# Performance work log

Hardware: AMD Instinct MI355X
Metric: run time of the kernel (lower is better)

The kernel has to match this reference:

```python
import jax, jax.numpy as jnp
import numpy as np

B, S, V = 2, 336, 8      # batch, seq_len, n_vars
D, H, P = 256, 8, 96     # d_model, num_heads, pred_len
DK = D // H
OUT_CHN = 8
EPS = 1e-5


def _layernorm(x, g, b):
    mu = jnp.mean(x, axis=-1, keepdims=True)
    var = jnp.var(x, axis=-1, keepdims=True)
    return (x - mu) * jax.lax.rsqrt(var + EPS) * g + b


def _attn_ff(src, Wq, bq, Wk, bk, Wv, bv, Wo, bo, ln1_g, ln1_b):
    # src: [N, L, D]; manual MHA + residual + layernorm (dropout=0)
    N, L, _ = src.shape
    q = (src @ Wq + bq).reshape(N, L, H, DK).transpose(0, 2, 1, 3)
    k = (src @ Wk + bk).reshape(N, L, H, DK).transpose(0, 2, 1, 3)
    v = (src @ Wv + bv).reshape(N, L, H, DK).transpose(0, 2, 1, 3)
    scores = jnp.einsum('nhqd,nhkd->nhqk', q, k) / np.sqrt(DK).astype(np.float32)
    attn = jax.nn.softmax(scores, axis=-1)
    o = jnp.einsum('nhqk,nhkd->nhqd', attn, v)
    o = o.transpose(0, 2, 1, 3).reshape(N, L, D) @ Wo + bo
    return _layernorm(src + o, ln1_g, ln1_b)


def setup_inputs() -> dict:
    key = jax.random.key(0)
    ks = jax.random.split(key, 8)
    s = 1.0 / np.sqrt(D)
    return {
        'x': jax.random.normal(ks[0], (B, S, V), dtype=jnp.float32),
        'emb_w': jax.random.normal(ks[1], (1, D), dtype=jnp.float32),
        'emb_b': jnp.zeros((D,), jnp.float32),
        'Wq': jax.random.normal(ks[2], (D, D), dtype=jnp.float32) * s,
        'bq': jnp.zeros((D,), jnp.float32),
        'Wk': jax.random.normal(ks[3], (D, D), dtype=jnp.float32) * s,
        'bk': jnp.zeros((D,), jnp.float32),
        'Wv': jax.random.normal(ks[4], (D, D), dtype=jnp.float32) * s,
        'bv': jnp.zeros((D,), jnp.float32),
        'Wo': jax.random.normal(ks[5], (D, D), dtype=jnp.float32) * s,
        'bo': jnp.zeros((D,), jnp.float32),
        'ln1_g': jnp.ones((D,), jnp.float32),
        'ln1_b': jnp.zeros((D,), jnp.float32),
        'norm_g': jnp.ones((D,), jnp.float32),
        'norm_b': jnp.zeros((D,), jnp.float32),
        'proj_w': jax.random.normal(ks[6], (S * D, P), dtype=jnp.float32) / np.sqrt(S * D).astype(np.float32),
        'proj_b': jnp.zeros((P,), jnp.float32),
    }


def reference(x, emb_w, emb_b, Wq, bq, Wk, bk, Wv, bv, Wo, bo,
              ln1_g, ln1_b, norm_g, norm_b, proj_w, proj_b):
    attn_p = (Wq, bq, Wk, bk, Wv, bv, Wo, bo, ln1_g, ln1_b)
    # x: [B,S,V] -> [B,V,S] -> embed each scalar to D
    e = x.transpose(0, 2, 1)[..., None] @ emb_w + emb_b  # [B,V,S,D]
    for _ in range(10):
        # attention over time axis (shared weights)
        e = _attn_ff(e.reshape(B * V, S, D), *attn_p).reshape(B, V, S, D)
        e = _layernorm(e.transpose(0, 2, 1, 3), norm_g, norm_b)  # [B,S,V,D]
        # attention over variable axis (same weights)
        e = _attn_ff(e.reshape(B * S, V, D), *attn_p).reshape(B, S, V, D)
        e = e.transpose(0, 2, 1, 3)  # [B,V,S,D]
    out = e.reshape(B, V, S * D) @ proj_w + proj_b  # [B,V,P]
    return out.transpose(0, 2, 1)[:, :, :OUT_CHN]  # [B,P,out_chn]
```

## Files before the change

### kernel.cpp

```cpp
#include <hip/hip_runtime.h>

#define SS 336
#define VV 8
#define DD 256
#define DKK 32
#define NTOK 5376
#define NTD (NTOK * DD)
#define ATT_SCALE 0.17677669529663687f
#define LN_EPS 1e-5f

typedef _Float16 f16x8 __attribute__((ext_vector_type(8)));
typedef _Float16 f16x4v __attribute__((ext_vector_type(4)));
typedef __attribute__((ext_vector_type(4))) float f32x4;

__device__ inline _Float16 f2h(float f) { return (_Float16)f; }

__global__ __launch_bounds__(256) void k_prep_w(
    const float* __restrict__ Wq, const float* __restrict__ Wk,
    const float* __restrict__ Wv, const float* __restrict__ Wo,
    _Float16* __restrict__ WT2) {
  int z = blockIdx.y;
  const float* W = (z == 0) ? Wq : (z == 1) ? Wk : (z == 2) ? Wv : Wo;
  int o = blockIdx.x * 256 + threadIdx.x;
  int blk = o >> 9;
  int idx = o & 511;
  int lane = idx >> 3, j = idx & 7;
  int nt = blk >> 3, kb = blk & 7;
  int lcol = lane & 15, quad = lane >> 4;
  int n = nt * 16 + lcol;
  int k = kb * 32 + quad * 8 + j;
  WT2[(size_t)z * 65536 + o] = f2h(W[k * 256 + n]);
}

__global__ __launch_bounds__(256) void k_embed(
    const float* __restrict__ x, const float* __restrict__ ew,
    const float* __restrict__ eb, float* __restrict__ E,
    _Float16* __restrict__ E16) {
  int token = blockIdx.x;
  int n = token / SS, s = token - n * SS;
  int b = n >> 3, v = n & 7;
  float xv = x[(b * SS + s) * VV + v];
  int d = threadIdx.x;
  float val = fmaf(xv, ew[d], eb[d]);
  E[token * DD + d] = val;
  E16[token * DD + d] = f2h(val);
}

__global__ __launch_bounds__(256) void k_gemm_qkv(
    const _Float16* __restrict__ A16, const _Float16* __restrict__ WT2,
    const float* __restrict__ c0, const float* __restrict__ c1,
    const float* __restrict__ c2,
    _Float16* __restrict__ H0, _Float16* __restrict__ H1,
    _Float16* __restrict__ H2) {
  int z = blockIdx.z;
  const float* bias = (z == 0) ? c0 : (z == 1) ? c1 : c2;
  _Float16* H       = (z == 0) ? H0 : (z == 1) ? H1 : H2;
  int m0 = blockIdx.x * 64;
  int tid = threadIdx.x;
  int wave = tid >> 6, lane = tid & 63;
  int wm = wave >> 1, wn = wave & 1;
  int quad = lane >> 4, lcol = lane & 15;
  int ntb = blockIdx.y * 8 + wn * 4;

  __shared__ _Float16 As[4 * 64 * 8];

  f32x4 acc[2][4] = {};

  for (int kb = 0; kb < 8; ++kb) {
    int k0 = kb * 32;
    __syncthreads();
    {
      int row = tid >> 2, ks = tid & 3;
      *(f16x8*)&As[(ks * 64 + row) * 8] =
          *(const f16x8*)&A16[(size_t)(m0 + row) * 256 + k0 + ks * 8];
    }
    __syncthreads();
    f16x8 af[2];
#pragma unroll
    for (int mt = 0; mt < 2; ++mt)
      af[mt] = *(const f16x8*)&As[(quad * 64 + wm * 32 + mt * 16 + lcol) * 8];
#pragma unroll
    for (int nt = 0; nt < 4; ++nt) {
      f16x8 bfr = *(const f16x8*)&WT2[(size_t)z * 65536 +
                                      ((ntb + nt) * 8 + kb) * 512 + lane * 8];
#pragma unroll
      for (int mt = 0; mt < 2; ++mt)
        acc[mt][nt] = __builtin_amdgcn_mfma_f32_16x16x32_f16(
            af[mt], bfr, acc[mt][nt], 0, 0, 0);
    }
  }

  float bsv[4];
#pragma unroll
  for (int nt = 0; nt < 4; ++nt) bsv[nt] = bias[(ntb + nt) * 16 + lcol];
#pragma unroll
  for (int mt = 0; mt < 2; ++mt) {
#pragma unroll
    for (int i = 0; i < 4; ++i) {
      int r = m0 + wm * 32 + mt * 16 + quad * 4 + i;
#pragma unroll
      for (int nt = 0; nt < 4; ++nt) {
        int c = (ntb + nt) * 16 + lcol;
        H[(size_t)r * 256 + c] = f2h(acc[mt][nt][i] + bsv[nt]);
      }
    }
  }
}

#define KSTR 36
#define VTSTR 344
__global__ __launch_bounds__(512) void k_attn_time(
    const _Float16* __restrict__ Q, const _Float16* __restrict__ K,
    const _Float16* __restrict__ V, _Float16* __restrict__ O16) {
  int qg = blockIdx.x, h = blockIdx.y, n = blockIdx.z;
  int tid = threadIdx.x;
  int wave = tid >> 6, lane = tid & 63;
  int quad = lane >> 4, lcol = lane & 15;

  __shared__ _Float16 Ks[336 * KSTR];
  __shared__ _Float16 Vt[32 * VTSTR + 16];
  __shared__ _Float16 Ps[8][16 * 40];

  const size_t base = (size_t)(n * SS) * DD + h * DKK;

  for (int c = tid; c < 1344; c += 512) {
    int row = c >> 2, part = c & 3;
    f16x8 kv = *(const f16x8*)&K[base + (size_t)row * DD + part * 8];
    f16x4v klo = __builtin_shufflevector(kv, kv, 0, 1, 2, 3);
    f16x4v khi = __builtin_shufflevector(kv, kv, 4, 5, 6, 7);
    *(f16x4v*)&Ks[row * KSTR + part * 8] = klo;
    *(f16x4v*)&Ks[row * KSTR + part * 8 + 4] = khi;
    f16x8 vv = *(const f16x8*)&V[base + (size_t)row * DD + part * 8];
#pragma unroll
    for (int j = 0; j < 8; ++j) Vt[(part * 8 + j) * VTSTR + row] = vv[j];
  }
  for (int c = tid; c < 272; c += 512) {
    if (c < 256) {
      int d = c >> 3, col = 336 + (c & 7);
      Vt[d * VTSTR + col] = (_Float16)0.f;
    } else {
      Vt[32 * VTSTR + (c - 256)] = (_Float16)0.f;
    }
  }
  __syncthreads();

  _Float16* P = Ps[wave];
  const f16x8 onesv = {(_Float16)1.f, (_Float16)1.f, (_Float16)1.f, (_Float16)1.f,
                       (_Float16)1.f, (_Float16)1.f, (_Float16)1.f, (_Float16)1.f};
  const f32x4 z4 = {0.f, 0.f, 0.f, 0.f};

  int qt0 = qg ? 11 : 0;
  int qtend = qg ? 21 : 11;
  for (int qtile = qt0 + wave; qtile < qtend; qtile += 8) {
    int qb = qtile * 16;

    f16x8 qf = *(const f16x8*)&Q[base + (size_t)(qb + lcol) * DD + quad * 8];
    f32x4 accA = {0.f, 0.f, 0.f, 0.f};
    f32x4 accB = {0.f, 0.f, 0.f, 0.f};
    f32x4 lacc = {0.f, 0.f, 0.f, 0.f};
    float m_[4] = {-1e30f, -1e30f, -1e30f, -1e30f};

    for (int t = 0; t < 11; ++t) {
      int k0 = t * 32;
      bool full = (t < 10);
      const _Float16* kp0 = &Ks[(k0 + lcol) * KSTR + quad * 8];
      f16x4v ka = *(const f16x4v*)kp0;
      f16x4v kb = *(const f16x4v*)(kp0 + 4);
      f16x8 kf0 = __builtin_shufflevector(ka, kb, 0, 1, 2, 3, 4, 5, 6, 7);
      f32x4 s0 = __builtin_amdgcn_mfma_f32_16x16x32_f16(qf, kf0, z4, 0, 0, 0);
      f32x4 s1 = z4;
      if (full) {
        const _Float16* kp1 = &Ks[(k0 + 16 + lcol) * KSTR + quad * 8];
        f16x4v ka1 = *(const f16x4v*)kp1;
        f16x4v kb1 = *(const f16x4v*)(kp1 + 4);
        f16x8 kf1 = __builtin_shufflevector(ka1, kb1, 0, 1, 2, 3, 4, 5, 6, 7);
        s1 = __builtin_amdgcn_mfma_f32_16x16x32_f16(qf, kf1, z4, 0, 0, 0);
      }
      float sc0[4], sc1[4], p0[4], p1[4], corr[4];
#pragma unroll
      for (int i = 0; i < 4; ++i) {
        sc0[i] = s0[i] * ATT_SCALE;
        sc1[i] = full ? s1[i] * ATT_SCALE : -1e30f;
      }
#pragma unroll
      for (int i = 0; i < 4; ++i) {
        float t2 = fmaxf(sc0[i], sc1[i]);
        t2 = fmaxf(t2, __shfl_xor(t2, 1));
        t2 = fmaxf(t2, __shfl_xor(t2, 2));
        t2 = fmaxf(t2, __shfl_xor(t2, 4));
        t2 = fmaxf(t2, __shfl_xor(t2, 8));
        float nm = fmaxf(m_[i], t2);
        corr[i] = __expf(m_[i] - nm);
        m_[i] = nm;
        p0[i] = __expf(sc0[i] - nm);
        p1[i] = __expf(sc1[i] - nm);
        accA[i] *= corr[i];
        accB[i] *= corr[i];
        lacc[i] *= corr[i];
      }
#pragma unroll
      for (int i = 0; i < 4; ++i) {
        P[(quad * 4 + i) * 40 + lcol] = f2h(p0[i]);
        P[(quad * 4 + i) * 40 + 16 + lcol] = f2h(p1[i]);
      }
      f16x8 pf = *(const f16x8*)&P[lcol * 40 + quad * 8];
      lacc = __builtin_amdgcn_mfma_f32_16x16x32_f16(pf, onesv, lacc, 0, 0, 0);
      f16x8 vb0 = *(const f16x8*)&Vt[lcol * VTSTR + k0 + quad * 8];
      f16x8 vb1 = *(const f16x8*)&Vt[(16 + lcol) * VTSTR + k0 + quad * 8];
      accA = __builtin_amdgcn_mfma_f32_16x16x32_f16(pf, vb0, accA, 0, 0, 0);
      accB = __builtin_amdgcn_mfma_f32_16x16x32_f16(pf, vb1, accB, 0, 0, 0);
    }

#pragma unroll
    for (int i = 0; i < 4; ++i) {
      float inv = 1.f / lacc[i];
      P[(quad * 4 + i) * 40 + lcol] = f2h(accA[i] * inv);
      P[(quad * 4 + i) * 40 + 16 + lcol] = f2h(accB[i] * inv);
    }
    int row = lane >> 2, seg = lane & 3;
    f16x8 ov = *(const f16x8*)&P[row * 40 + seg * 8];
    *(f16x8*)&O16[base + (size_t)(qb + row) * DD + seg * 8] = ov;
  }
}

__global__ __launch_bounds__(512) void k_mega_var(
    const _Float16* __restrict__ AO16, const _Float16* __restrict__ WT2,
    const float* __restrict__ bq, const float* __restrict__ bk,
    const float* __restrict__ bv, const float* __restrict__ bo,
    const float* __restrict__ g1, const float* __restrict__ c1,
    const float* __restrict__ gn, const float* __restrict__ bn,
    float* __restrict__ Etime, _Float16* __restrict__ Q16,
    _Float16* __restrict__ K16, _Float16* __restrict__ V16, int doqkv) {
  int tid = threadIdx.x;
  int wave = tid >> 6, lane = tid & 63;
  int quad = lane >> 4, lcol = lane & 15;

  __shared__ int rmapS[32];
  __shared__ _Float16 Af[32 * 264];
  __shared__ float Cf[32 * 260];
  __shared__ _Float16 QKVs[32 * 776];

  if (tid < 32) {
    int r2 = blockIdx.x * 32 + tid;
    int n_idx = r2 >> 3, v = r2 & 7;
    int b = n_idx / SS, s = n_idx - b * SS;
    rmapS[tid] = (b * VV + v) * SS + s;
  }
  __syncthreads();

  {
    int row = tid >> 4, seg = tid & 15;
    const _Float16* src = AO16 + (size_t)rmapS[row] * DD + seg * 16;
    _Float16* dst = Af + row * 264 + seg * 16;
    *(f16x8*)(dst) = *(const f16x8*)(src);
    *(f16x8*)(dst + 8) = *(const f16x8*)(src + 8);
  }
  __syncthreads();

  const _Float16* WoF = WT2 + (size_t)3 * 65536;

  {
    f32x4 acc[2][2] = {};
    for (int kb = 0; kb < 8; ++kb) {
      int k0 = kb * 32;
      f16x8 af0 = *(const f16x8*)&Af[lcol * 264 + k0 + quad * 8];
      f16x8 af1 = *(const f16x8*)&Af[(16 + lcol) * 264 + k0 + quad * 8];
#pragma unroll
      for (int nt = 0; nt < 2; ++nt) {
        f16x8 bfr = *(const f16x8*)&WoF[((wave * 2 + nt) * 8 + kb) * 512 + lane * 8];
        acc[0][nt] = __builtin_amdgcn_mfma_f32_16x16x32_f16(af0, bfr, acc[0][nt], 0, 0, 0);
        acc[1][nt] = __builtin_amdgcn_mfma_f32_16x16x32_f16(af1, bfr, acc[1][nt], 0, 0, 0);
      }
    }
#pragma unroll
    for (int mt = 0; mt < 2; ++mt) {
#pragma unroll
      for (int i = 0; i < 4; ++i) {
        int row = mt * 16 + quad * 4 + i;
        size_t rb = (size_t)rmapS[row] * 256;
#pragma unroll
        for (int nt = 0; nt < 2; ++nt) {
          int col = (wave * 2 + nt) * 16 + lcol;
          Cf[row * 260 + col] = acc[mt][nt][i] + bo[col] + Etime[rb + col];
        }
      }
    }
  }
  __syncthreads();

  {
    int row = tid >> 4, c0 = (tid & 15) * 16;
    float v[16];
#pragma unroll
    for (int j = 0; j < 16; ++j) v[j] = Cf[row * 260 + c0 + j];
#pragma unroll
    for (int pass = 0; pass < 2; ++pass) {
      const float* gg = pass ? gn : g1;
      const float* bb = pass ? bn : c1;
      float s = 0.f, q = 0.f;
#pragma unroll
      for (int j = 0; j < 16; ++j) { s += v[j]; q = fmaf(v[j], v[j], q); }
      s += __shfl_xor(s, 1); q += __shfl_xor(q, 1);
      s += __shfl_xor(s, 2); q += __shfl_xor(q, 2);
      s += __shfl_xor(s, 4); q += __shfl_xor(q, 4);
      s += __shfl_xor(s, 8); q += __shfl_xor(q, 8);
      float mu = s * (1.0f / 256.0f);
      float rs = rsqrtf(q * (1.0f / 256.0f) - mu * mu + LN_EPS);
#pragma unroll
      for (int j = 0; j < 16; ++j)
        v[j] = fmaf((v[j] - mu) * rs, gg[c0 + j], bb[c0 + j]);
    }
#pragma unroll
    for (int j = 0; j < 16; ++j) Cf[row * 260 + c0 + j] = v[j];
#pragma unroll
    for (int j8 = 0; j8 < 2; ++j8) {
      f16x8 h;
#pragma unroll
      for (int jj = 0; jj < 8; ++jj) h[jj] = f2h(v[j8 * 8 + jj]);
      *(f16x8*)&Af[row * 264 + c0 + j8 * 8] = h;
    }
  }
  __syncthreads();

  {
    f32x4 acc[2][6] = {};
    for (int kb = 0; kb < 8; ++kb) {
      int k0 = kb * 32;
      f16x8 af0 = *(const f16x8*)&Af[lcol * 264 + k0 + quad * 8];
      f16x8 af1 = *(const f16x8*)&Af[(16 + lcol) * 264 + k0 + quad * 8];
#pragma unroll
      for (int j = 0; j < 6; ++j) {
        int ntg = wave * 6 + j;
        f16x8 bfr = *(const f16x8*)&WT2[(size_t)(ntg * 8 + kb) * 512 + lane * 8];
        acc[0][j] = __builtin_amdgcn_mfma_f32_16x16x32_f16(af0, bfr, acc[0][j], 0, 0, 0);
        acc[1][j] = __builtin_amdgcn_mfma_f32_16x16x32_f16(af1, bfr, acc[1][j], 0, 0, 0);
      }
    }
#pragma unroll
    for (int j = 0; j < 6; ++j) {
      int ntg = wave * 6 + j;
      int colb = ntg * 16;
      int z = colb >> 8, coln = (colb & 255) + lcol;
      const float* bz = (z == 0) ? bq : (z == 1) ? bk : bv;
      float bval = bz[coln];
#pragma unroll
      for (int mt = 0; mt < 2; ++mt) {
#pragma unroll
        for (int i = 0; i < 4; ++i)
          QKVs[(mt * 16 + quad * 4 + i) * 776 + colb + lcol] = f2h(acc[mt][j][i] + bval);
      }
    }
  }
  __syncthreads();

  if (tid < 256) {
    int ng = tid >> 6, h = (tid >> 3) & 7, qi = tid & 7;
    const _Float16* Qp = &QKVs[(ng * 8 + qi) * 776 + h * 32];
    float qv[32];
#pragma unroll
    for (int j4 = 0; j4 < 4; ++j4) {
      f16x8 t = *(const f16x8*)(Qp + j4 * 8);
#pragma unroll
      for (int jj = 0; jj < 8; ++jj) qv[j4 * 8 + jj] = (float)t[jj];
    }
    float sc[8];
#pragma unroll
    for (int k = 0; k < 8; ++k) {
      const _Float16* Kp = &QKVs[(ng * 8 + k) * 776 + 256 + h * 32];
      float s = 0.f;
#pragma unroll
      for (int j4 = 0; j4 < 4; ++j4) {
        f16x8 t = *(const f16x8*)(Kp + j4 * 8);
#pragma unroll
        for (int jj = 0; jj < 8; ++jj) s = fmaf(qv[j4 * 8 + jj], (float)t[jj], s);
      }
      sc[k] = s * ATT_SCALE;
    }
    float mx = sc[0];
#pragma unroll
    for (int k = 1; k < 8; ++k) mx = fmaxf(mx, sc[k]);
    float ps = 0.f;
#pragma unroll
    for (int k = 0; k < 8; ++k) { sc[k] = __expf(sc[k] - mx); ps += sc[k]; }
    float inv = 1.f / ps;
    float ov[32];
#pragma unroll
    for (int j = 0; j < 32; ++j) ov[j] = 0.f;
#pragma unroll
    for (int k = 0; k < 8; ++k) {
      const _Float16* Vp = &QKVs[(ng * 8 + k) * 776 + 512 + h * 32];
      float p = sc[k];
#pragma unroll
      for (int j4 = 0; j4 < 4; ++j4) {
        f16x8 t = *(const f16x8*)(Vp + j4 * 8);
#pragma unroll
        for (int jj = 0; jj < 8; ++jj)
          ov[j4 * 8 + jj] = fmaf(p, (float)t[jj], ov[j4 * 8 + jj]);
      }
    }
    _Float16* Op = &Af[(ng * 8 + qi) * 264 + h * 32];
#pragma unroll
    for (int j4 = 0; j4 < 4; ++j4) {
      f16x8 hh;
#pragma unroll
      for (int jj = 0; jj < 8; ++jj) hh[jj] = f2h(ov[j4 * 8 + jj] * inv);
      *(f16x8*)(Op + j4 * 8) = hh;
    }
  }
  __syncthreads();

  {
    f32x4 acc[2][2] = {};
    for (int kb = 0; kb < 8; ++kb) {
      int k0 = kb * 32;
      f16x8 af0 = *(const f16x8*)&Af[lcol * 264 + k0 + quad * 8];
      f16x8 af1 = *(const f16x8*)&Af[(16 + lcol) * 264 + k0 + quad * 8];
#pragma unroll
      for (int nt = 0; nt < 2; ++nt) {
        f16x8 bfr = *(const f16x8*)&WoF[((wave * 2 + nt) * 8 + kb) * 512 + lane * 8];
        acc[0][nt] = __builtin_amdgcn_mfma_f32_16x16x32_f16(af0, bfr, acc[0][nt], 0, 0, 0);
        acc[1][nt] = __builtin_amdgcn_mfma_f32_16x16x32_f16(af1, bfr, acc[1][nt], 0, 0, 0);
      }
    }
#pragma unroll
    for (int mt = 0; mt < 2; ++mt) {
#pragma unroll
      for (int i = 0; i < 4; ++i) {
        int row = mt * 16 + quad * 4 + i;
#pragma unroll
        for (int nt = 0; nt < 2; ++nt) {
          int col = (wave * 2 + nt) * 16 + lcol;
          Cf[row * 260 + col] = acc[mt][nt][i] + bo[col] + Cf[row * 260 + col];
        }
      }
    }
  }
  __syncthreads();

  {
    int row = tid >> 4, c0 = (tid & 15) * 16;
    float v[16];
#pragma unroll
    for (int j = 0; j < 16; ++j) v[j] = Cf[row * 260 + c0 + j];
    float s = 0.f, q = 0.f;
#pragma unroll
    for (int j = 0; j < 16; ++j) { s += v[j]; q = fmaf(v[j], v[j], q); }
    s += __shfl_xor(s, 1); q += __shfl_xor(q, 1);
    s += __shfl_xor(s, 2); q += __shfl_xor(q, 2);
    s += __shfl_xor(s, 4); q += __shfl_xor(q, 4);
    s += __shfl_xor(s, 8); q += __shfl_xor(q, 8);
    float mu = s * (1.0f / 256.0f);
    float rs = rsqrtf(q * (1.0f / 256.0f) - mu * mu + LN_EPS);
#pragma unroll
    for (int j = 0; j < 16; ++j)
      v[j] = fmaf((v[j] - mu) * rs, g1[c0 + j], c1[c0 + j]);
    size_t rb = (size_t)rmapS[row] * 256 + c0;
#pragma unroll
    for (int j4 = 0; j4 < 4; ++j4) {
      float4 f4 = make_float4(v[j4 * 4], v[j4 * 4 + 1], v[j4 * 4 + 2], v[j4 * 4 + 3]);
      *(float4*)&Etime[rb + j4 * 4] = f4;
    }
#pragma unroll
    for (int j8 = 0; j8 < 2; ++j8) {
      f16x8 hh;
#pragma unroll
      for (int jj = 0; jj < 8; ++jj) hh[jj] = f2h(v[j8 * 8 + jj]);
      *(f16x8*)&Af[row * 264 + c0 + j8 * 8] = hh;
    }
  }
  __syncthreads();

  if (doqkv) {
    f32x4 acc[2][6] = {};
    for (int kb = 0; kb < 8; ++kb) {
      int k0 = kb * 32;
      f16x8 af0 = *(const f16x8*)&Af[lcol * 264 + k0 + quad * 8];
      f16x8 af1 = *(const f16x8*)&Af[(16 + lcol) * 264 + k0 + quad * 8];
#pragma unroll
      for (int j = 0; j < 6; ++j) {
        int ntg = wave * 6 + j;
        f16x8 bfr = *(const f16x8*)&WT2[(size_t)(ntg * 8 + kb) * 512 + lane * 8];
        acc[0][j] = __builtin_amdgcn_mfma_f32_16x16x32_f16(af0, bfr, acc[0][j], 0, 0, 0);
        acc[1][j] = __builtin_amdgcn_mfma_f32_16x16x32_f16(af1, bfr, acc[1][j], 0, 0, 0);
      }
    }
#pragma unroll
    for (int j = 0; j < 6; ++j) {
      int ntg = wave * 6 + j;
      int colb = ntg * 16;
      int z = colb >> 8, coln = (colb & 255) + lcol;
      const float* bz = (z == 0) ? bq : (z == 1) ? bk : bv;
      _Float16* Hd = (z == 0) ? Q16 : (z == 1) ? K16 : V16;
      float bval = bz[coln];
#pragma unroll
      for (int mt = 0; mt < 2; ++mt) {
#pragma unroll
        for (int i = 0; i < 4; ++i) {
          int row = mt * 16 + quad * 4 + i;
          Hd[(size_t)rmapS[row] * 256 + coln] = f2h(acc[mt][j][i] + bval);
        }
      }
    }
  }
}

__global__ __launch_bounds__(192) void k_proj_partial(
    const float* __restrict__ E, const float* __restrict__ PW,
    float* __restrict__ Part) {
  int kc = blockIdx.x;
  int tid = threadIdx.x;
  int p4 = tid % 24, g = tid / 24;
  __shared__ float Es[16][128];
  __shared__ float sm[8][1536];
  for (int idx = tid; idx < 512; idx += 192) {
    int row = idx >> 5, kk4 = idx & 31;
    *(float4*)&Es[row][kk4 * 4] =
        *(const float4*)&E[(size_t)row * 86016 + kc * 128 + kk4 * 4];
  }
  __syncthreads();
  float4 acc[16];
#pragma unroll
  for (int i = 0; i < 16; ++i) acc[i] = make_float4(0.f, 0.f, 0.f, 0.f);
  for (int j = 0; j < 16; ++j) {
    int k = g * 16 + j;
    float4 w = *(const float4*)&PW[(size_t)(kc * 128 + k) * 96 + p4 * 4];
#pragma unroll
    for (int row = 0; row < 16; ++row) {
      float e = Es[row][k];
      acc[row].x = fmaf(e, w.x, acc[row].x);
      acc[row].y = fmaf(e, w.y, acc[row].y);
      acc[row].z = fmaf(e, w.z, acc[row].z);
      acc[row].w = fmaf(e, w.w, acc[row].w);
    }
  }
#pragma unroll
  for (int row = 0; row < 16; ++row)
    *(float4*)&sm[g][row * 96 + p4 * 4] = acc[row];
  __syncthreads();
  for (int o = tid; o < 1536; o += 192) {
    float s = 0.f;
#pragma unroll
    for (int g2 = 0; g2 < 8; ++g2) s += sm[g2][o];
    Part[(size_t)kc * 1536 + o] = s;
  }
}

__global__ __launch_bounds__(256) void k_proj_reduce(
    const float* __restrict__ Part, const float* __restrict__ PB,
    float* __restrict__ out) {
  int j = blockIdx.x * 256 + threadIdx.x;
  int row = j / 96, p = j - row * 96;
  float s = PB[p];
#pragma unroll 8
  for (int c = 0; c < 672; ++c) s += Part[(size_t)c * 1536 + j];
  int b = row >> 3, v = row & 7;
  out[b * 768 + p * 8 + v] = s;
}

extern "C" void kernel_launch(void* const* d_in, const int* in_sizes, int n_in,
                              void* d_out, int out_size, void* d_ws,
                              size_t ws_size, hipStream_t stream) {
  const float* x     = (const float*)d_in[0];
  const float* emb_w = (const float*)d_in[1];
  const float* emb_b = (const float*)d_in[2];
  const float* Wq = (const float*)d_in[3];
  const float* bq = (const float*)d_in[4];
  const float* Wk = (const float*)d_in[5];
  const float* bk = (const float*)d_in[6];
  const float* Wv = (const float*)d_in[7];
  const float* bv = (const float*)d_in[8];
  const float* Wo = (const float*)d_in[9];
  const float* bo = (const float*)d_in[10];
  const float* g1 = (const float*)d_in[11];
  const float* b1 = (const float*)d_in[12];
  const float* gn = (const float*)d_in[13];
  const float* bn = (const float*)d_in[14];
  const float* PW = (const float*)d_in[15];
  const float* PB = (const float*)d_in[16];
  float* out = (float*)d_out;

  float* ws = (float*)d_ws;
  float* Etime   = ws;
  _Float16* Et16 = (_Float16*)(ws + (size_t)NTD);
  _Float16* Q16  = (_Float16*)(ws + (size_t)NTD + NTD / 2);
  _Float16* K16  = Q16 + (size_t)NTD;
  _Float16* V16  = K16 + (size_t)NTD;
  _Float16* AO16 = V16 + (size_t)NTD;
  _Float16* WT2  = AO16 + (size_t)NTD;
  float* Part    = (float*)(WT2 + 4 * 65536);

  k_prep_w<<<dim3(256, 4), 256, 0, stream>>>(Wq, Wk, Wv, Wo, WT2);
  k_embed<<<NTOK, 256, 0, stream>>>(x, emb_w, emb_b, Etime, Et16);
  k_gemm_qkv<<<dim3(84, 2, 3), 256, 0, stream>>>(
      Et16, WT2, bq, bk, bv, Q16, K16, V16);
  for (int it = 0; it < 10; ++it) {
    k_attn_time<<<dim3(2, 8, 16), 512, 0, stream>>>(Q16, K16, V16, AO16);
    k_mega_var<<<168, 512, 0, stream>>>(
        AO16, WT2, bq, bk, bv, bo, g1, b1, gn, bn, Etime,
        Q16, K16, V16, (it < 9) ? 1 : 0);
  }
  k_proj_partial<<<672, 192, 0, stream>>>(Etime, PW, Part);
  k_proj_reduce<<<6, 256, 0, stream>>>(Part, PB, out);
}
```

Before: 595.8 us.

## Retune QKV GEMM staging, time-attention tiles, var-attention split and projection reduce

Four independent changes. The QKV GEMM now stages the whole 64x256 A tile in shared memory once, replacing the two barriers per k-step. Time attention processes 64 keys per softmax step instead of 32, halving the online-softmax max/rescale passes. The variable-axis attention splits each head's 32-dim dot products across two threads (all 512 threads active, combined with a shuffle). The projection reduce is spread over 96 blocks with a split-K shared-memory reduction instead of 6 blocks looping serially over 672 partials. The costs are more shared memory and register pressure, and the reduce's summation order changes.

```diff
diff --git a/kernel.cpp b/kernel.cpp
--- a/kernel.cpp
+++ b/kernel.cpp
@@ -62,23 +62,23 @@
   int quad = lane >> 4, lcol = lane & 15;
   int ntb = blockIdx.y * 8 + wn * 4;
 
-  __shared__ _Float16 As[4 * 64 * 8];
+  __shared__ _Float16 As[64 * 264];
+
+  for (int c = tid; c < 2048; c += 256) {
+    int row = c >> 5, seg = c & 31;
+    *(f16x8*)&As[row * 264 + seg * 8] =
+        *(const f16x8*)&A16[(size_t)(m0 + row) * 256 + seg * 8];
+  }
+  __syncthreads();
 
   f32x4 acc[2][4] = {};
 
   for (int kb = 0; kb < 8; ++kb) {
     int k0 = kb * 32;
-    __syncthreads();
-    {
-      int row = tid >> 2, ks = tid & 3;
-      *(f16x8*)&As[(ks * 64 + row) * 8] =
-          *(const f16x8*)&A16[(size_t)(m0 + row) * 256 + k0 + ks * 8];
-    }
-    __syncthreads();
     f16x8 af[2];
 #pragma unroll
     for (int mt = 0; mt < 2; ++mt)
-      af[mt] = *(const f16x8*)&As[(quad * 64 + wm * 32 + mt * 16 + lcol) * 8];
+      af[mt] = *(const f16x8*)&As[(wm * 32 + mt * 16 + lcol) * 264 + k0 + quad * 8];
 #pragma unroll
     for (int nt = 0; nt < 4; ++nt) {
       f16x8 bfr = *(const f16x8*)&WT2[(size_t)z * 65536 +
@@ -109,6 +109,7 @@
 
 #define KSTR 36
 #define VTSTR 344
+#define PSTR 72
 __global__ __launch_bounds__(512) void k_attn_time(
     const _Float16* __restrict__ Q, const _Float16* __restrict__ K,
     const _Float16* __restrict__ V, _Float16* __restrict__ O16) {
@@ -119,7 +120,7 @@
 
   __shared__ _Float16 Ks[336 * KSTR];
   __shared__ _Float16 Vt[32 * VTSTR + 16];
-  __shared__ _Float16 Ps[8][16 * 40];
+  __shared__ _Float16 Ps[8][16 * PSTR];
 
   const size_t base = (size_t)(n * SS) * DD + h * DKK;
 
@@ -160,31 +161,38 @@
     f32x4 lacc = {0.f, 0.f, 0.f, 0.f};
     float m_[4] = {-1e30f, -1e30f, -1e30f, -1e30f};
 
-    for (int t = 0; t < 11; ++t) {
-      int k0 = t * 32;
-      bool full = (t < 10);
-      const _Float16* kp0 = &Ks[(k0 + lcol) * KSTR + quad * 8];
-      f16x4v ka = *(const f16x4v*)kp0;
-      f16x4v kb = *(const f16x4v*)(kp0 + 4);
-      f16x8 kf0 = __builtin_shufflevector(ka, kb, 0, 1, 2, 3, 4, 5, 6, 7);
-      f32x4 s0 = __builtin_amdgcn_mfma_f32_16x16x32_f16(qf, kf0, z4, 0, 0, 0);
-      f32x4 s1 = z4;
+    for (int T = 0; T < 6; ++T) {
+      int k0 = T * 64;
+      bool full = (T < 5);
+      f32x4 s[4];
+      {
+        const _Float16* kp = &Ks[(k0 + lcol) * KSTR + quad * 8];
+        f16x4v a0 = *(const f16x4v*)kp;
+        f16x4v b0 = *(const f16x4v*)(kp + 4);
+        f16x8 kf = __builtin_shufflevector(a0, b0, 0, 1, 2, 3, 4, 5, 6, 7);
+        s[0] = __builtin_amdgcn_mfma_f32_16x16x32_f16(qf, kf, z4, 0, 0, 0);
+      }
       if (full) {
-        const _Float16* kp1 = &Ks[(k0 + 16 + lcol) * KSTR + quad * 8];
-        f16x4v ka1 = *(const f16x4v*)kp1;
-        f16x4v kb1 = *(const f16x4v*)(kp1 + 4);
-        f16x8 kf1 = __builtin_shufflevector(ka1, kb1, 0, 1, 2, 3, 4, 5, 6, 7);
-        s1 = __builtin_amdgcn_mfma_f32_16x16x32_f16(qf, kf1, z4, 0, 0, 0);
-      }
-      float sc0[4], sc1[4], p0[4], p1[4], corr[4];
+#pragma unroll
+        for (int u = 1; u < 4; ++u) {
+          const _Float16* kp = &Ks[(k0 + u * 16 + lcol) * KSTR + quad * 8];
+          f16x4v a0 = *(const f16x4v*)kp;
+          f16x4v b0 = *(const f16x4v*)(kp + 4);
+          f16x8 kf = __builtin_shufflevector(a0, b0, 0, 1, 2, 3, 4, 5, 6, 7);
+          s[u] = __builtin_amdgcn_mfma_f32_16x16x32_f16(qf, kf, z4, 0, 0, 0);
+        }
+      } else {
+        s[1] = z4; s[2] = z4; s[3] = z4;
+      }
+      float sc[4][4], p[4][4], corr[4];
+#pragma unroll
+      for (int u = 0; u < 4; ++u)
+#pragma unroll
+        for (int i = 0; i < 4; ++i)
+          sc[u][i] = (u == 0 || full) ? s[u][i] * ATT_SCALE : -1e30f;
 #pragma unroll
       for (int i = 0; i < 4; ++i) {
-        sc0[i] = s0[i] * ATT_SCALE;
-        sc1[i] = full ? s1[i] * ATT_SCALE : -1e30f;
-      }
-#pragma unroll
-      for (int i = 0; i < 4; ++i) {
-        float t2 = fmaxf(sc0[i], sc1[i]);
+        float t2 = fmaxf(fmaxf(sc[0][i], sc[1][i]), fmaxf(sc[2][i], sc[3][i]));
         t2 = fmaxf(t2, __shfl_xor(t2, 1));
         t2 = fmaxf(t2, __shfl_xor(t2, 2));
         t2 = fmaxf(t2, __shfl_xor(t2, 4));
@@ -192,33 +200,41 @@
         float nm = fmaxf(m_[i], t2);
         corr[i] = __expf(m_[i] - nm);
         m_[i] = nm;
-        p0[i] = __expf(sc0[i] - nm);
-        p1[i] = __expf(sc1[i] - nm);
+#pragma unroll
+        for (int u = 0; u < 4; ++u) p[u][i] = __expf(sc[u][i] - nm);
         accA[i] *= corr[i];
         accB[i] *= corr[i];
         lacc[i] *= corr[i];
       }
 #pragma unroll
-      for (int i = 0; i < 4; ++i) {
-        P[(quad * 4 + i) * 40 + lcol] = f2h(p0[i]);
-        P[(quad * 4 + i) * 40 + 16 + lcol] = f2h(p1[i]);
-      }
-      f16x8 pf = *(const f16x8*)&P[lcol * 40 + quad * 8];
-      lacc = __builtin_amdgcn_mfma_f32_16x16x32_f16(pf, onesv, lacc, 0, 0, 0);
-      f16x8 vb0 = *(const f16x8*)&Vt[lcol * VTSTR + k0 + quad * 8];
-      f16x8 vb1 = *(const f16x8*)&Vt[(16 + lcol) * VTSTR + k0 + quad * 8];
-      accA = __builtin_amdgcn_mfma_f32_16x16x32_f16(pf, vb0, accA, 0, 0, 0);
-      accB = __builtin_amdgcn_mfma_f32_16x16x32_f16(pf, vb1, accB, 0, 0, 0);
+      for (int i = 0; i < 4; ++i)
+#pragma unroll
+        for (int u = 0; u < 4; ++u)
+          P[(quad * 4 + i) * PSTR + u * 16 + lcol] = f2h(p[u][i]);
+      f16x8 pf0 = *(const f16x8*)&P[lcol * PSTR + quad * 8];
+      lacc = __builtin_amdgcn_mfma_f32_16x16x32_f16(pf0, onesv, lacc, 0, 0, 0);
+      f16x8 va0 = *(const f16x8*)&Vt[lcol * VTSTR + k0 + quad * 8];
+      f16x8 vb0 = *(const f16x8*)&Vt[(16 + lcol) * VTSTR + k0 + quad * 8];
+      accA = __builtin_amdgcn_mfma_f32_16x16x32_f16(pf0, va0, accA, 0, 0, 0);
+      accB = __builtin_amdgcn_mfma_f32_16x16x32_f16(pf0, vb0, accB, 0, 0, 0);
+      if (full) {
+        f16x8 pf1 = *(const f16x8*)&P[lcol * PSTR + 32 + quad * 8];
+        lacc = __builtin_amdgcn_mfma_f32_16x16x32_f16(pf1, onesv, lacc, 0, 0, 0);
+        f16x8 va1 = *(const f16x8*)&Vt[lcol * VTSTR + k0 + 32 + quad * 8];
+        f16x8 vb1 = *(const f16x8*)&Vt[(16 + lcol) * VTSTR + k0 + 32 + quad * 8];
+        accA = __builtin_amdgcn_mfma_f32_16x16x32_f16(pf1, va1, accA, 0, 0, 0);
+        accB = __builtin_amdgcn_mfma_f32_16x16x32_f16(pf1, vb1, accB, 0, 0, 0);
+      }
     }
 
 #pragma unroll
     for (int i = 0; i < 4; ++i) {
       float inv = 1.f / lacc[i];
-      P[(quad * 4 + i) * 40 + lcol] = f2h(accA[i] * inv);
-      P[(quad * 4 + i) * 40 + 16 + lcol] = f2h(accB[i] * inv);
+      P[(quad * 4 + i) * PSTR + lcol] = f2h(accA[i] * inv);
+      P[(quad * 4 + i) * PSTR + 16 + lcol] = f2h(accB[i] * inv);
     }
     int row = lane >> 2, seg = lane & 3;
-    f16x8 ov = *(const f16x8*)&P[row * 40 + seg * 8];
+    f16x8 ov = *(const f16x8*)&P[row * PSTR + seg * 8];
     *(f16x8*)&O16[base + (size_t)(qb + row) * DD + seg * 8] = ov;
   }
 }
@@ -353,29 +369,33 @@
   }
   __syncthreads();
 
-  if (tid < 256) {
-    int ng = tid >> 6, h = (tid >> 3) & 7, qi = tid & 7;
-    const _Float16* Qp = &QKVs[(ng * 8 + qi) * 776 + h * 32];
-    float qv[32];
-#pragma unroll
-    for (int j4 = 0; j4 < 4; ++j4) {
-      f16x8 t = *(const f16x8*)(Qp + j4 * 8);
-#pragma unroll
-      for (int jj = 0; jj < 8; ++jj) qv[j4 * 8 + jj] = (float)t[jj];
+  {
+    int half = tid & 1, qi = (tid >> 1) & 7, h = (tid >> 4) & 7, ng = tid >> 7;
+    int d0 = h * 32 + half * 16;
+    const _Float16* Qp = &QKVs[(ng * 8 + qi) * 776 + d0];
+    float qv[16];
+#pragma unroll
+    for (int j8 = 0; j8 < 2; ++j8) {
+      f16x8 t = *(const f16x8*)(Qp + j8 * 8);
+#pragma unroll
+      for (int jj = 0; jj < 8; ++jj) qv[j8 * 8 + jj] = (float)t[jj];
     }
     float sc[8];
 #pragma unroll
     for (int k = 0; k < 8; ++k) {
-      const _Float16* Kp = &QKVs[(ng * 8 + k) * 776 + 256 + h * 32];
+      const _Float16* Kp = &QKVs[(ng * 8 + k) * 776 + 256 + d0];
       float s = 0.f;
 #pragma unroll
-      for (int j4 = 0; j4 < 4; ++j4) {
-        f16x8 t = *(const f16x8*)(Kp + j4 * 8);
-#pragma unroll
-        for (int jj = 0; jj < 8; ++jj) s = fmaf(qv[j4 * 8 + jj], (float)t[jj], s);
-      }
-      sc[k] = s * ATT_SCALE;
-    }
+      for (int j8 = 0; j8 < 2; ++j8) {
+        f16x8 t = *(const f16x8*)(Kp + j8 * 8);
+#pragma unroll
+        for (int jj = 0; jj < 8; ++jj) s = fmaf(qv[j8 * 8 + jj], (float)t[jj], s);
+      }
+      sc[k] = s;
+    }
+#pragma unroll
+    for (int k = 0; k < 8; ++k)
+      sc[k] = (sc[k] + __shfl_xor(sc[k], 1)) * ATT_SCALE;
     float mx = sc[0];
 #pragma unroll
     for (int k = 1; k < 8; ++k) mx = fmaxf(mx, sc[k]);
@@ -383,28 +403,28 @@
 #pragma unroll
     for (int k = 0; k < 8; ++k) { sc[k] = __expf(sc[k] - mx); ps += sc[k]; }
     float inv = 1.f / ps;
-    float ov[32];
-#pragma unroll
-    for (int j = 0; j < 32; ++j) ov[j] = 0.f;
+    float ov[16];
+#pragma unroll
+    for (int j = 0; j < 16; ++j) ov[j] = 0.f;
 #pragma unroll
     for (int k = 0; k < 8; ++k) {
-      const _Float16* Vp = &QKVs[(ng * 8 + k) * 776 + 512 + h * 32];
+      const _Float16* Vp = &QKVs[(ng * 8 + k) * 776 + 512 + d0];
       float p = sc[k];
 #pragma unroll
-      for (int j4 = 0; j4 < 4; ++j4) {
-        f16x8 t = *(const f16x8*)(Vp + j4 * 8);
+      for (int j8 = 0; j8 < 2; ++j8) {
+        f16x8 t = *(const f16x8*)(Vp + j8 * 8);
 #pragma unroll
         for (int jj = 0; jj < 8; ++jj)
-          ov[j4 * 8 + jj] = fmaf(p, (float)t[jj], ov[j4 * 8 + jj]);
-      }
-    }
-    _Float16* Op = &Af[(ng * 8 + qi) * 264 + h * 32];
-#pragma unroll
-    for (int j4 = 0; j4 < 4; ++j4) {
+          ov[j8 * 8 + jj] = fmaf(p, (float)t[jj], ov[j8 * 8 + jj]);
+      }
+    }
+    _Float16* Op = &Af[(ng * 8 + qi) * 264 + d0];
+#pragma unroll
+    for (int j8 = 0; j8 < 2; ++j8) {
       f16x8 hh;
 #pragma unroll
-      for (int jj = 0; jj < 8; ++jj) hh[jj] = f2h(ov[j4 * 8 + jj] * inv);
-      *(f16x8*)(Op + j4 * 8) = hh;
+      for (int jj = 0; jj < 8; ++jj) hh[jj] = f2h(ov[j8 * 8 + jj] * inv);
+      *(f16x8*)(Op + j8 * 8) = hh;
     }
   }
   __syncthreads();
@@ -548,13 +568,28 @@
 __global__ __launch_bounds__(256) void k_proj_reduce(
     const float* __restrict__ Part, const float* __restrict__ PB,
     float* __restrict__ out) {
-  int j = blockIdx.x * 256 + threadIdx.x;
-  int row = j / 96, p = j - row * 96;
-  float s = PB[p];
-#pragma unroll 8
-  for (int c = 0; c < 672; ++c) s += Part[(size_t)c * 1536 + j];
-  int b = row >> 3, v = row & 7;
-  out[b * 768 + p * 8 + v] = s;
+  __shared__ float red[4][16];
+  int tid = threadIdx.x;
+  int j = (blockIdx.x << 4) | (tid & 15);
+  int cg = tid >> 4;
+  float s = 0.f;
+#pragma unroll 7
+  for (int i = 0; i < 42; ++i) {
+    int c = cg * 42 + i;
+    s += Part[(size_t)c * 1536 + j];
+  }
+  s += __shfl_xor(s, 16);
+  s += __shfl_xor(s, 32);
+  int wv = tid >> 6;
+  if ((tid & 63) < 16) red[wv][tid & 15] = s;
+  __syncthreads();
+  if (tid < 16) {
+    float t = red[0][tid] + red[1][tid] + red[2][tid] + red[3][tid];
+    int jj = (blockIdx.x << 4) | tid;
+    int row = jj / 96, p = jj - row * 96;
+    int b = row >> 3, v = row & 7;
+    out[b * 768 + p * 8 + v] = PB[p] + t;
+  }
 }
 
 extern "C" void kernel_launch(void* const* d_in, const int* in_sizes, int n_in,
@@ -600,5 +635,5 @@
         Q16, K16, V16, (it < 9) ? 1 : 0);
   }
   k_proj_partial<<<672, 192, 0, stream>>>(Etime, PW, Part);
-  k_proj_reduce<<<6, 256, 0, stream>>>(Part, PB, out);
-}
+  k_proj_reduce<<<96, 256, 0, stream>>>(Part, PB, out);
+}
```

Result: faster. 571.8 us (-4.0%).
